# Kernel optimization log

Hardware: AMD Instinct MI355X
Metric: run time of the kernel (lower is better)

The kernel has to match this reference:

```python
import jax, jax.numpy as jnp
import numpy as np
from math import gcd

KAISER_BETA = 5.0  # scipy resample_poly default window=('kaiser', 5.0)


def _firwin_kaiser(numtaps, cutoff, beta):
    # lowpass firwin equivalent: windowed-sinc, normalized to unity DC gain
    m = np.arange(numtaps) - (numtaps - 1) / 2.0
    h = cutoff * np.sinc(cutoff * m)
    h *= np.kaiser(numtaps, beta)
    h /= h.sum()
    return h


def _output_len(len_h, in_len, up, down):
    # full upfirdn output length
    return ((in_len - 1) * up + len_h - 1) // down + 1


def _make_filter(du, su, n_in):
    # replicates scipy.signal.resample_poly filter design + zero padding
    g = gcd(su, du)
    up, down = su // g, du // g
    max_rate = max(up, down)
    half_len = 10 * max_rate
    h = _firwin_kaiser(2 * half_len + 1, 1.0 / max_rate, KAISER_BETA) * up
    n_pre_pad = down - half_len % down
    n_out = n_in * up // down + bool((n_in * up) % down)
    n_pre_remove = (half_len + n_pre_pad) // down
    n_post_pad = 0
    while _output_len(len(h) + n_pre_pad + n_post_pad, n_in, up, down) < n_out + n_pre_remove:
        n_post_pad += 1
    h = np.concatenate([np.zeros(n_pre_pad), h, np.zeros(n_post_pad)]).astype(np.float32)
    return h


B, T, C = 16, 1_280_000, 4


def setup_inputs() -> dict:
    key = jax.random.key(0)
    x = jax.random.normal(key, (B, T, C), dtype=jnp.float32)
    h = jnp.asarray(_make_filter(640, 50, T))  # [1345]
    return {"x": x, "h": h, "su": 50, "du": 640}


def reference(x, h, su, du):
    # polyphase resampling: upsample by `up` (lhs_dilation), FIR filter h
    # (full convolution), downsample by `down` (stride) == scipy upfirdn,
    # then trim transients exactly as scipy.signal.resample_poly does.
    Bx, Tx, Cx = x.shape
    g = gcd(su, du)
    up, down = su // g, du // g  # 5, 64
    half_len = 10 * max(up, down)
    n_pre_pad = down - half_len % down
    n_pre_remove = (half_len + n_pre_pad) // down
    n_out = Tx * up // down + bool((Tx * up) % down)
    K = h.shape[0]
    # resample along time axis (axis=1): [B, T, C] -> [B*C, 1, T]
    xc = jnp.transpose(x, (0, 2, 1)).reshape(Bx * Cx, 1, Tx)
    kern = h[::-1].reshape(1, 1, K).astype(x.dtype)  # flip: conv, not corr
    y = jax.lax.conv_general_dilated(
        xc, kern,
        window_strides=(down,),
        padding=[(K - 1, K - 1)],
        lhs_dilation=(up,),
        dimension_numbers=("NCH", "OIH", "NCH"),
    )  # [B*C, 1, L_full]
    y = y[:, 0, n_pre_remove:n_pre_remove + n_out]
    return jnp.transpose(y.reshape(Bx, Cx, n_out), (0, 2, 1))  # [B, n_out, C]
```

## Files before the change

### kernel.cpp

```cpp
#include <hip/hip_runtime.h>

#define T_IN    1280000
#define N_OUT   100000
#define NQ      20000
#define KH      1345
#define NKP     352
#define QT      64
#define NTILE   313
#define LOW_PAD 163
#define SPAN    4388
#define PLANE_BYTES 18640
#define LDS_BYTES   74560

__global__ void build_tables(const float* __restrict__ h, float* __restrict__ ws) {
    int k = blockIdx.x * blockDim.x + threadIdx.x;
    if (k >= NKP) return;
    int m0 = 5 * k - 256;
    float4* tab4 = (float4*)ws;
    float*  tab1 = ws + NKP * 4;
    float v0 = (m0       >= 0 && m0       < KH) ? h[m0]       : 0.0f;
    float v1 = (m0 + 64  >= 0 && m0 + 64  < KH) ? h[m0 + 64]  : 0.0f;
    float v2 = (m0 + 128 >= 0 && m0 + 128 < KH) ? h[m0 + 128] : 0.0f;
    float v3 = (m0 + 192 >= 0 && m0 + 192 < KH) ? h[m0 + 192] : 0.0f;
    float v4 = (m0 + 256 >= 0 && m0 + 256 < KH) ? h[m0 + 256] : 0.0f;
    tab4[k] = make_float4(v0, v1, v2, v3);
    tab1[k] = v4;
}

#define STEP(T, TB, CMP) \
  a0.x = fmaf(T.x, xq0.CMP, a0.x); a0.y = fmaf(T.x, xq1.CMP, a0.y); \
  a0.z = fmaf(T.x, xq2.CMP, a0.z); a0.w = fmaf(T.x, xq3.CMP, a0.w); \
  a1.x = fmaf(T.y, xq0.CMP, a1.x); a1.y = fmaf(T.y, xq1.CMP, a1.y); \
  a1.z = fmaf(T.y, xq2.CMP, a1.z); a1.w = fmaf(T.y, xq3.CMP, a1.w); \
  a2.x = fmaf(T.z, xq0.CMP, a2.x); a2.y = fmaf(T.z, xq1.CMP, a2.y); \
  a2.z = fmaf(T.z, xq2.CMP, a2.z); a2.w = fmaf(T.z, xq3.CMP, a2.w); \
  a3.x = fmaf(T.w, xq0.CMP, a3.x); a3.y = fmaf(T.w, xq1.CMP, a3.y); \
  a3.z = fmaf(T.w, xq2.CMP, a3.z); a3.w = fmaf(T.w, xq3.CMP, a3.w); \
  a4.x = fmaf(TB,  xq0.CMP, a4.x); a4.y = fmaf(TB,  xq1.CMP, a4.y); \
  a4.z = fmaf(TB,  xq2.CMP, a4.z); a4.w = fmaf(TB,  xq3.CMP, a4.w);

__launch_bounds__(512, 4)
__global__ void downsample_poly(const float* __restrict__ x,
                                const float* __restrict__ ws,
                                float* __restrict__ out) {
    extern __shared__ __align__(16) unsigned char lds_raw[];
    const int tid = threadIdx.x;
    const int b   = blockIdx.y;
    const int q0  = blockIdx.x * QT;
    const int jlo = 64 * q0 - LOW_PAD;

    const float4* __restrict__ xb = (const float4*)x + (size_t)b * T_IN;

    for (int i = tid; i < SPAN; i += 512) {
        int j = jlo + i;
        float4 v = make_float4(0.f, 0.f, 0.f, 0.f);
        if ((unsigned)j < (unsigned)T_IN) v = xb[j];
        int G    = i >> 2;
        int slot = G + (G >> 4);
        int base = slot * 16 + (i & 3) * 4;
        *(float*)(lds_raw + base)                   = v.x;
        *(float*)(lds_raw + base +     PLANE_BYTES) = v.y;
        *(float*)(lds_raw + base + 2 * PLANE_BYTES) = v.z;
        *(float*)(lds_raw + base + 3 * PLANE_BYTES) = v.w;
    }
    __syncthreads();

    const int dq = tid & 63;
    const int su = __builtin_amdgcn_readfirstlane(tid >> 6);
    const float4* __restrict__ tap4 = (const float4*)ws;
    const float*  __restrict__ tap1 = ws + NKP * 4;

    float4 a0 = make_float4(0.f,0.f,0.f,0.f), a1 = a0, a2 = a0, a3 = a0, a4 = a0;
    const int k00 = su * 44;
    const int Gb0 = 16 * dq + 88 - 11 * su;

    #pragma unroll 2
    for (int g = 0; g < 11; ++g) {
        int k0   = k00 + 4 * g;
        int Gb   = Gb0 - g;
        int slot = Gb + (Gb >> 4);
        const unsigned char* pb = lds_raw + slot * 16;
        float4 xq0 = *(const float4*)(pb);
        float4 xq1 = *(const float4*)(pb +     PLANE_BYTES);
        float4 xq2 = *(const float4*)(pb + 2 * PLANE_BYTES);
        float4 xq3 = *(const float4*)(pb + 3 * PLANE_BYTES);
        float4 t0 = tap4[k0], t1 = tap4[k0 + 1], t2 = tap4[k0 + 2], t3 = tap4[k0 + 3];
        float4 u1 = *(const float4*)(tap1 + k0);
        STEP(t0, u1.x, w)
        STEP(t1, u1.y, z)
        STEP(t2, u1.z, y)
        STEP(t3, u1.w, x)
    }

    __syncthreads();
    {
        float4* pp = (float4*)(lds_raw + tid * 80);
        pp[0] = a0; pp[1] = a1; pp[2] = a2; pp[3] = a3; pp[4] = a4;
    }
    __syncthreads();
    if (tid < 320 && 5 * q0 + tid < 5 * NQ) {
        float sx = 0.f, sy = 0.f, sz = 0.f, sw = 0.f;
        #pragma unroll
        for (int ss = 0; ss < 8; ++ss) {
            float4 p = *(const float4*)(lds_raw + ss * 5120 + tid * 16);
            sx += p.x; sy += p.y; sz += p.z; sw += p.w;
        }
        ((float4*)out)[(size_t)b * N_OUT + 5 * (size_t)q0 + tid] =
            make_float4(sx, sy, sz, sw);
    }
}

extern "C" void kernel_launch(void* const* d_in, const int* in_sizes, int n_in,
                              void* d_out, int out_size, void* d_ws, size_t ws_size,
                              hipStream_t stream) {
    const float* x = (const float*)d_in[0];
    const float* h = (const float*)d_in[1];
    float* out = (float*)d_out;
    float* ws  = (float*)d_ws;

    hipFuncSetAttribute((const void*)downsample_poly,
                        hipFuncAttributeMaxDynamicSharedMemorySize, LDS_BYTES);

    hipLaunchKernelGGL(build_tables, dim3(2), dim3(192), 0, stream, h, ws);
    hipLaunchKernelGGL(downsample_poly, dim3(NTILE, 16), dim3(512), LDS_BYTES,
                       stream, x, ws, out);
}
```

Baseline: 458.6 us.

## Stage input in fp16 LDS and use packed fdot2 for polyphase taps

Converts the staged input and filter taps to packed fp16 pairs and replaces the fp32 FMA chains with v_dot2 (fdot2) accumulating into fp32. This halves LDS footprint, which allows static shared memory, an XOR swizzle instead of padded slots, and a launch bound of 8 waves per SIMD target. It aims to cut ALU instruction count and LDS traffic. The trade-off is reduced precision of input and taps from round-toward-zero fp16 conversion, which may exceed tolerance.

```diff
diff --git a/kernel.cpp b/kernel.cpp
--- a/kernel.cpp
+++ b/kernel.cpp
@@ -1,112 +1,113 @@
 #include <hip/hip_runtime.h>
 
-#define T_IN    1280000
-#define N_OUT   100000
-#define NQ      20000
-#define KH      1345
-#define NKP     352
-#define QT      64
-#define NTILE   313
-#define LOW_PAD 163
-#define SPAN    4388
-#define PLANE_BYTES 18640
-#define LDS_BYTES   74560
+typedef _Float16 h2 __attribute__((ext_vector_type(2)));
+typedef _Float16 h4 __attribute__((ext_vector_type(4)));
 
-__global__ void build_tables(const float* __restrict__ h, float* __restrict__ ws) {
-    int k = blockIdx.x * blockDim.x + threadIdx.x;
-    if (k >= NKP) return;
-    int m0 = 5 * k - 256;
-    float4* tab4 = (float4*)ws;
-    float*  tab1 = ws + NKP * 4;
-    float v0 = (m0       >= 0 && m0       < KH) ? h[m0]       : 0.0f;
-    float v1 = (m0 + 64  >= 0 && m0 + 64  < KH) ? h[m0 + 64]  : 0.0f;
-    float v2 = (m0 + 128 >= 0 && m0 + 128 < KH) ? h[m0 + 128] : 0.0f;
-    float v3 = (m0 + 192 >= 0 && m0 + 192 < KH) ? h[m0 + 192] : 0.0f;
-    float v4 = (m0 + 256 >= 0 && m0 + 256 < KH) ? h[m0 + 256] : 0.0f;
-    tab4[k] = make_float4(v0, v1, v2, v3);
-    tab1[k] = v4;
+#define T_IN   1280000
+#define N_OUT  100000
+#define NQ     20000
+#define KH     1345
+#define NMP    176
+#define QT     64
+#define NTILE  313
+#define OFFJ   159
+#define NPAIR  2240
+#define PLANE  9216
+#define SWZ(b) ((b) ^ ((((b) >> 7) & 15) << 3))
+#define PKRTZ(a, b) __builtin_bit_cast(h2, __builtin_amdgcn_cvt_pkrtz((a), (b)))
+
+__global__ void build_tables(const float* __restrict__ h, unsigned* __restrict__ ws) {
+    int m = blockIdx.x * blockDim.x + threadIdx.x;
+    if (m >= NMP) return;
+    #pragma unroll
+    for (int r = 0; r < 5; ++r) {
+        int ilo = 5 * (2 * m)     - 256 + 64 * r;
+        int ihi = 5 * (2 * m + 1) - 256 + 64 * r;
+        float vlo = (ilo >= 0 && ilo < KH) ? h[ilo] : 0.f;
+        float vhi = (ihi >= 0 && ihi < KH) ? h[ihi] : 0.f;
+        h2 p = PKRTZ(vhi, vlo);
+        ws[m * 5 + r] = __builtin_bit_cast(unsigned, p);
+    }
 }
 
-#define STEP(T, TB, CMP) \
-  a0.x = fmaf(T.x, xq0.CMP, a0.x); a0.y = fmaf(T.x, xq1.CMP, a0.y); \
-  a0.z = fmaf(T.x, xq2.CMP, a0.z); a0.w = fmaf(T.x, xq3.CMP, a0.w); \
-  a1.x = fmaf(T.y, xq0.CMP, a1.x); a1.y = fmaf(T.y, xq1.CMP, a1.y); \
-  a1.z = fmaf(T.y, xq2.CMP, a1.z); a1.w = fmaf(T.y, xq3.CMP, a1.w); \
-  a2.x = fmaf(T.z, xq0.CMP, a2.x); a2.y = fmaf(T.z, xq1.CMP, a2.y); \
-  a2.z = fmaf(T.z, xq2.CMP, a2.z); a2.w = fmaf(T.z, xq3.CMP, a2.w); \
-  a3.x = fmaf(T.w, xq0.CMP, a3.x); a3.y = fmaf(T.w, xq1.CMP, a3.y); \
-  a3.z = fmaf(T.w, xq2.CMP, a3.z); a3.w = fmaf(T.w, xq3.CMP, a3.w); \
-  a4.x = fmaf(TB,  xq0.CMP, a4.x); a4.y = fmaf(TB,  xq1.CMP, a4.y); \
-  a4.z = fmaf(TB,  xq2.CMP, a4.z); a4.w = fmaf(TB,  xq3.CMP, a4.w);
+#define DOT_R(AR, TH, TL) \
+  AR.x = __builtin_amdgcn_fdot2(TH, Xl0, AR.x, false); \
+  AR.x = __builtin_amdgcn_fdot2(TL, Xh0, AR.x, false); \
+  AR.y = __builtin_amdgcn_fdot2(TH, Xl1, AR.y, false); \
+  AR.y = __builtin_amdgcn_fdot2(TL, Xh1, AR.y, false); \
+  AR.z = __builtin_amdgcn_fdot2(TH, Xl2, AR.z, false); \
+  AR.z = __builtin_amdgcn_fdot2(TL, Xh2, AR.z, false); \
+  AR.w = __builtin_amdgcn_fdot2(TH, Xl3, AR.w, false); \
+  AR.w = __builtin_amdgcn_fdot2(TL, Xh3, AR.w, false);
 
-__launch_bounds__(512, 4)
+__launch_bounds__(512, 8)
 __global__ void downsample_poly(const float* __restrict__ x,
-                                const float* __restrict__ ws,
+                                const unsigned* __restrict__ ws,
                                 float* __restrict__ out) {
-    extern __shared__ __align__(16) unsigned char lds_raw[];
+    __shared__ __align__(16) char lds[40960];
     const int tid = threadIdx.x;
     const int b   = blockIdx.y;
     const int q0  = blockIdx.x * QT;
-    const int jlo = 64 * q0 - LOW_PAD;
-
+    const int jlo = 64 * q0 - OFFJ;
     const float4* __restrict__ xb = (const float4*)x + (size_t)b * T_IN;
 
-    for (int i = tid; i < SPAN; i += 512) {
-        int j = jlo + i;
-        float4 v = make_float4(0.f, 0.f, 0.f, 0.f);
-        if ((unsigned)j < (unsigned)T_IN) v = xb[j];
-        int G    = i >> 2;
-        int slot = G + (G >> 4);
-        int base = slot * 16 + (i & 3) * 4;
-        *(float*)(lds_raw + base)                   = v.x;
-        *(float*)(lds_raw + base +     PLANE_BYTES) = v.y;
-        *(float*)(lds_raw + base + 2 * PLANE_BYTES) = v.z;
-        *(float*)(lds_raw + base + 3 * PLANE_BYTES) = v.w;
+    #pragma unroll
+    for (int it = 0; it < 5; ++it) {
+        int i2 = tid + it * 512;
+        if (i2 < NPAIR) {
+            int j0 = jlo + 2 * i2;
+            float4 v0 = make_float4(0.f, 0.f, 0.f, 0.f), v1 = v0;
+            if ((unsigned)j0       < (unsigned)T_IN) v0 = xb[j0];
+            if ((unsigned)(j0 + 1) < (unsigned)T_IN) v1 = xb[j0 + 1];
+            int bb = SWZ(4 * i2);
+            *(h2*)(lds + bb)             = PKRTZ(v0.x, v1.x);
+            *(h2*)(lds + bb +     PLANE) = PKRTZ(v0.y, v1.y);
+            *(h2*)(lds + bb + 2 * PLANE) = PKRTZ(v0.z, v1.z);
+            *(h2*)(lds + bb + 3 * PLANE) = PKRTZ(v0.w, v1.w);
+        }
     }
     __syncthreads();
 
     const int dq = tid & 63;
     const int su = __builtin_amdgcn_readfirstlane(tid >> 6);
-    const float4* __restrict__ tap4 = (const float4*)ws;
-    const float*  __restrict__ tap1 = ws + NKP * 4;
-
     float4 a0 = make_float4(0.f,0.f,0.f,0.f), a1 = a0, a2 = a0, a3 = a0, a4 = a0;
-    const int k00 = su * 44;
-    const int Gb0 = 16 * dq + 88 - 11 * su;
+    const int rb0 = 128 * dq + 696 - 88 * su;
 
     #pragma unroll 2
     for (int g = 0; g < 11; ++g) {
-        int k0   = k00 + 4 * g;
-        int Gb   = Gb0 - g;
-        int slot = Gb + (Gb >> 4);
-        const unsigned char* pb = lds_raw + slot * 16;
-        float4 xq0 = *(const float4*)(pb);
-        float4 xq1 = *(const float4*)(pb +     PLANE_BYTES);
-        float4 xq2 = *(const float4*)(pb + 2 * PLANE_BYTES);
-        float4 xq3 = *(const float4*)(pb + 3 * PLANE_BYTES);
-        float4 t0 = tap4[k0], t1 = tap4[k0 + 1], t2 = tap4[k0 + 2], t3 = tap4[k0 + 3];
-        float4 u1 = *(const float4*)(tap1 + k0);
-        STEP(t0, u1.x, w)
-        STEP(t1, u1.y, z)
-        STEP(t2, u1.z, y)
-        STEP(t3, u1.w, x)
+        int sw = SWZ(rb0 - 8 * g);
+        h4 X0 = *(const h4*)(lds + sw);
+        h4 X1 = *(const h4*)(lds + sw +     PLANE);
+        h4 X2 = *(const h4*)(lds + sw + 2 * PLANE);
+        h4 X3 = *(const h4*)(lds + sw + 3 * PLANE);
+        h2 Xl0 = {X0[0], X0[1]}, Xh0 = {X0[2], X0[3]};
+        h2 Xl1 = {X1[0], X1[1]}, Xh1 = {X1[2], X1[3]};
+        h2 Xl2 = {X2[0], X2[1]}, Xh2 = {X2[2], X2[3]};
+        h2 Xl3 = {X3[0], X3[1]}, Xh3 = {X3[2], X3[3]};
+        const unsigned* tw = ws + (110 * su + 10 * g);
+        h2 th, tl;
+        th = __builtin_bit_cast(h2, tw[5]); tl = __builtin_bit_cast(h2, tw[0]); DOT_R(a0, th, tl)
+        th = __builtin_bit_cast(h2, tw[6]); tl = __builtin_bit_cast(h2, tw[1]); DOT_R(a1, th, tl)
+        th = __builtin_bit_cast(h2, tw[7]); tl = __builtin_bit_cast(h2, tw[2]); DOT_R(a2, th, tl)
+        th = __builtin_bit_cast(h2, tw[8]); tl = __builtin_bit_cast(h2, tw[3]); DOT_R(a3, th, tl)
+        th = __builtin_bit_cast(h2, tw[9]); tl = __builtin_bit_cast(h2, tw[4]); DOT_R(a4, th, tl)
     }
 
     __syncthreads();
     {
-        float4* pp = (float4*)(lds_raw + tid * 80);
+        float4* pp = (float4*)(lds + tid * 80);
         pp[0] = a0; pp[1] = a1; pp[2] = a2; pp[3] = a3; pp[4] = a4;
     }
     __syncthreads();
     if (tid < 320 && 5 * q0 + tid < 5 * NQ) {
-        float sx = 0.f, sy = 0.f, sz = 0.f, sw = 0.f;
+        float sx = 0.f, sy = 0.f, sz = 0.f, sw2 = 0.f;
         #pragma unroll
         for (int ss = 0; ss < 8; ++ss) {
-            float4 p = *(const float4*)(lds_raw + ss * 5120 + tid * 16);
-            sx += p.x; sy += p.y; sz += p.z; sw += p.w;
+            float4 p = *(const float4*)(lds + ss * 5120 + tid * 16);
+            sx += p.x; sy += p.y; sz += p.z; sw2 += p.w;
         }
         ((float4*)out)[(size_t)b * N_OUT + 5 * (size_t)q0 + tid] =
-            make_float4(sx, sy, sz, sw);
+            make_float4(sx, sy, sz, sw2);
     }
 }
 
@@ -116,12 +117,9 @@
     const float* x = (const float*)d_in[0];
     const float* h = (const float*)d_in[1];
     float* out = (float*)d_out;
-    float* ws  = (float*)d_ws;
+    unsigned* ws = (unsigned*)d_ws;
 
-    hipFuncSetAttribute((const void*)downsample_poly,
-                        hipFuncAttributeMaxDynamicSharedMemorySize, LDS_BYTES);
-
-    hipLaunchKernelGGL(build_tables, dim3(2), dim3(192), 0, stream, h, ws);
-    hipLaunchKernelGGL(downsample_poly, dim3(NTILE, 16), dim3(512), LDS_BYTES,
-                       stream, x, ws, out);
+    hipLaunchKernelGGL(build_tables, dim3(1), dim3(192), 0, stream, h, ws);
+    hipLaunchKernelGGL(downsample_poly, dim3(NTILE, 16), dim3(512), 0, stream,
+                       x, ws, out);
 }
```

Measured after the change: 449.5 us. 1.02x faster.

## Use persistent blocks with double-buffered async global-to-LDS DMA and swizzled layout

Applied to the files above, without the earlier changes.

Replaces the one-block-per-tile grid with 256 persistent blocks that loop over tiles. Each block prefetches the next tile's input straight into LDS with global_load_lds while it computes the current one, so load latency overlaps compute. The LDS layout moves from channel-split planes to an XOR-swizzled float4 layout, and edge tiles get explicit zero fill. The cost is twice the LDS per block, lower occupancy, and hand-placed waitcnt and barrier ordering that is easy to get wrong.

```diff
diff --git a/kernel.cpp b/kernel.cpp
--- a/kernel.cpp
+++ b/kernel.cpp
@@ -1,16 +1,19 @@
 #include <hip/hip_runtime.h>
 
-#define T_IN    1280000
-#define N_OUT   100000
-#define NQ      20000
-#define KH      1345
-#define NKP     352
-#define QT      64
-#define NTILE   313
-#define LOW_PAD 163
-#define SPAN    4388
-#define PLANE_BYTES 18640
-#define LDS_BYTES   74560
+
+#define T_IN   1280000
+#define N_OUT  100000
+#define NQ     20000
+#define KH     1345
+#define NKP    352
+#define NTILE  313
+#define NTASK  5008
+#define GRID   256
+#define OFFJ   159
+#define SPAN   4480
+#define NCHUNK 70
+#define BUFB   71680
+#define LDSSZ  143360
 
 __global__ void build_tables(const float* __restrict__ h, float* __restrict__ ws) {
     int k = blockIdx.x * blockDim.x + threadIdx.x;
@@ -27,86 +30,114 @@
     tab1[k] = v4;
 }
 
-#define STEP(T, TB, CMP) \
-  a0.x = fmaf(T.x, xq0.CMP, a0.x); a0.y = fmaf(T.x, xq1.CMP, a0.y); \
-  a0.z = fmaf(T.x, xq2.CMP, a0.z); a0.w = fmaf(T.x, xq3.CMP, a0.w); \
-  a1.x = fmaf(T.y, xq0.CMP, a1.x); a1.y = fmaf(T.y, xq1.CMP, a1.y); \
-  a1.z = fmaf(T.y, xq2.CMP, a1.z); a1.w = fmaf(T.y, xq3.CMP, a1.w); \
-  a2.x = fmaf(T.z, xq0.CMP, a2.x); a2.y = fmaf(T.z, xq1.CMP, a2.y); \
-  a2.z = fmaf(T.z, xq2.CMP, a2.z); a2.w = fmaf(T.z, xq3.CMP, a2.w); \
-  a3.x = fmaf(T.w, xq0.CMP, a3.x); a3.y = fmaf(T.w, xq1.CMP, a3.y); \
-  a3.z = fmaf(T.w, xq2.CMP, a3.z); a3.w = fmaf(T.w, xq3.CMP, a3.w); \
-  a4.x = fmaf(TB,  xq0.CMP, a4.x); a4.y = fmaf(TB,  xq1.CMP, a4.y); \
-  a4.z = fmaf(TB,  xq2.CMP, a4.z); a4.w = fmaf(TB,  xq3.CMP, a4.w);
+#define FMA20(T, TB, XV) \
+  a0.x = fmaf(T.x, XV.x, a0.x); a0.y = fmaf(T.x, XV.y, a0.y); \
+  a0.z = fmaf(T.x, XV.z, a0.z); a0.w = fmaf(T.x, XV.w, a0.w); \
+  a1.x = fmaf(T.y, XV.x, a1.x); a1.y = fmaf(T.y, XV.y, a1.y); \
+  a1.z = fmaf(T.y, XV.z, a1.z); a1.w = fmaf(T.y, XV.w, a1.w); \
+  a2.x = fmaf(T.z, XV.x, a2.x); a2.y = fmaf(T.z, XV.y, a2.y); \
+  a2.z = fmaf(T.z, XV.z, a2.z); a2.w = fmaf(T.z, XV.w, a2.w); \
+  a3.x = fmaf(T.w, XV.x, a3.x); a3.y = fmaf(T.w, XV.y, a3.y); \
+  a3.z = fmaf(T.w, XV.z, a3.z); a3.w = fmaf(T.w, XV.w, a3.w); \
+  a4.x = fmaf(TB,  XV.x, a4.x); a4.y = fmaf(TB,  XV.y, a4.y); \
+  a4.z = fmaf(TB,  XV.z, a4.z); a4.w = fmaf(TB,  XV.w, a4.w);
 
-__launch_bounds__(512, 4)
+#define WAIT_VM8   asm volatile("s_waitcnt vmcnt(8)" ::: "memory")
+#define WAIT_LGKM0 asm volatile("s_waitcnt lgkmcnt(0)" ::: "memory")
+#define BAR() { __builtin_amdgcn_sched_barrier(0); __builtin_amdgcn_s_barrier(); \
+                __builtin_amdgcn_sched_barrier(0); }
+
+typedef const __attribute__((address_space(1))) void* gas_t;
+typedef __attribute__((address_space(3))) void* las_t;
+
+#define ISSUE_DMA(UU, BUFP) { \
+    int bb_ = (UU) / NTILE; \
+    int tt_ = (UU) - bb_ * NTILE; \
+    int jlo_ = (tt_ << 12) - OFFJ; \
+    const float4* __restrict__ xb_ = (const float4*)x + (size_t)bb_ * T_IN; \
+    for (int c_ = wid; c_ < NCHUNK; c_ += 8) { \
+        int j_ = jlo_ + (c_ << 6) + (lane ^ (c_ & 7)); \
+        j_ = j_ < 0 ? 0 : (j_ >= T_IN ? T_IN - 1 : j_); \
+        __builtin_amdgcn_global_load_lds((gas_t)(xb_ + j_), \
+                                         (las_t)((BUFP) + (c_ << 10)), 16, 0, 0); \
+    } }
+
+__launch_bounds__(512, 2)
 __global__ void downsample_poly(const float* __restrict__ x,
                                 const float* __restrict__ ws,
                                 float* __restrict__ out) {
-    extern __shared__ __align__(16) unsigned char lds_raw[];
-    const int tid = threadIdx.x;
-    const int b   = blockIdx.y;
-    const int q0  = blockIdx.x * QT;
-    const int jlo = 64 * q0 - LOW_PAD;
-
-    const float4* __restrict__ xb = (const float4*)x + (size_t)b * T_IN;
-
-    for (int i = tid; i < SPAN; i += 512) {
-        int j = jlo + i;
-        float4 v = make_float4(0.f, 0.f, 0.f, 0.f);
-        if ((unsigned)j < (unsigned)T_IN) v = xb[j];
-        int G    = i >> 2;
-        int slot = G + (G >> 4);
-        int base = slot * 16 + (i & 3) * 4;
-        *(float*)(lds_raw + base)                   = v.x;
-        *(float*)(lds_raw + base +     PLANE_BYTES) = v.y;
-        *(float*)(lds_raw + base + 2 * PLANE_BYTES) = v.z;
-        *(float*)(lds_raw + base + 3 * PLANE_BYTES) = v.w;
-    }
-    __syncthreads();
-
-    const int dq = tid & 63;
-    const int su = __builtin_amdgcn_readfirstlane(tid >> 6);
+    extern __shared__ __align__(16) char lds[];
+    const int tid  = threadIdx.x;
+    const int lane = tid & 63;
+    const int wid  = __builtin_amdgcn_readfirstlane(tid >> 6);
+    const int dq   = lane;
+    const int su   = wid;
     const float4* __restrict__ tap4 = (const float4*)ws;
     const float*  __restrict__ tap1 = ws + NKP * 4;
+    const int mbase = 64 * dq + 348 - 44 * su;
 
-    float4 a0 = make_float4(0.f,0.f,0.f,0.f), a1 = a0, a2 = a0, a3 = a0, a4 = a0;
-    const int k00 = su * 44;
-    const int Gb0 = 16 * dq + 88 - 11 * su;
+    int u = blockIdx.x;
+    ISSUE_DMA(u, lds)
 
-    #pragma unroll 2
-    for (int g = 0; g < 11; ++g) {
-        int k0   = k00 + 4 * g;
-        int Gb   = Gb0 - g;
-        int slot = Gb + (Gb >> 4);
-        const unsigned char* pb = lds_raw + slot * 16;
-        float4 xq0 = *(const float4*)(pb);
-        float4 xq1 = *(const float4*)(pb +     PLANE_BYTES);
-        float4 xq2 = *(const float4*)(pb + 2 * PLANE_BYTES);
-        float4 xq3 = *(const float4*)(pb + 3 * PLANE_BYTES);
-        float4 t0 = tap4[k0], t1 = tap4[k0 + 1], t2 = tap4[k0 + 2], t3 = tap4[k0 + 3];
-        float4 u1 = *(const float4*)(tap1 + k0);
-        STEP(t0, u1.x, w)
-        STEP(t1, u1.y, z)
-        STEP(t2, u1.z, y)
-        STEP(t3, u1.w, x)
-    }
+    for (int it = 0; u < NTASK; u += GRID, ++it) {
+        char* bufC = lds + ((it & 1) ? BUFB : 0);
+        char* bufN = lds + ((it & 1) ? 0 : BUFB);
+        int un = u + GRID; if (un >= NTASK) un = u;
+        ISSUE_DMA(un, bufN)
 
-    __syncthreads();
-    {
-        float4* pp = (float4*)(lds_raw + tid * 80);
-        pp[0] = a0; pp[1] = a1; pp[2] = a2; pp[3] = a3; pp[4] = a4;
-    }
-    __syncthreads();
-    if (tid < 320 && 5 * q0 + tid < 5 * NQ) {
-        float sx = 0.f, sy = 0.f, sz = 0.f, sw = 0.f;
-        #pragma unroll
-        for (int ss = 0; ss < 8; ++ss) {
-            float4 p = *(const float4*)(lds_raw + ss * 5120 + tid * 16);
-            sx += p.x; sy += p.y; sz += p.z; sw += p.w;
+        WAIT_VM8;
+        BAR();
+
+        const int bb  = u / NTILE;
+        const int tt  = u - bb * NTILE;
+        const int jlo = (tt << 12) - OFFJ;
+        int lo_bad = jlo < 0 ? -jlo : 0;
+        int hi_bad = T_IN - jlo; if (hi_bad > SPAN) hi_bad = SPAN;
+        if (lo_bad > 0 || hi_bad < SPAN) {
+            for (int m = tid; m < SPAN; m += 512)
+                if (m < lo_bad || m >= hi_bad)
+                    *(float4*)(bufC + ((m ^ ((m >> 6) & 7)) << 4)) =
+                        make_float4(0.f, 0.f, 0.f, 0.f);
+            WAIT_LGKM0; BAR();
         }
-        ((float4*)out)[(size_t)b * N_OUT + 5 * (size_t)q0 + tid] =
-            make_float4(sx, sy, sz, sw);
+
+        float4 a0 = make_float4(0.f,0.f,0.f,0.f), a1 = a0, a2 = a0, a3 = a0, a4 = a0;
+        for (int g = 0; g < 11; ++g) {
+            int m  = mbase - 4 * g;
+            int xr = (m >> 6) & 7;
+            float4 X0 = *(const float4*)(bufC + (((m    ) ^ xr) << 4));
+            float4 X1 = *(const float4*)(bufC + (((m + 1) ^ xr) << 4));
+            float4 X2 = *(const float4*)(bufC + (((m + 2) ^ xr) << 4));
+            float4 X3 = *(const float4*)(bufC + (((m + 3) ^ xr) << 4));
+            int k0 = 44 * su + 4 * g;
+            float4 t0 = tap4[k0], t1 = tap4[k0+1], t2 = tap4[k0+2], t3 = tap4[k0+3];
+            float4 u1 = *(const float4*)(tap1 + k0);
+            FMA20(t3, u1.w, X0)
+            FMA20(t2, u1.z, X1)
+            FMA20(t1, u1.y, X2)
+            FMA20(t0, u1.x, X3)
+        }
+
+        WAIT_LGKM0; BAR();
+        {
+            float4* pp = (float4*)(bufC + tid * 80);
+            pp[0] = a0; pp[1] = a1; pp[2] = a2; pp[3] = a3; pp[4] = a4;
+        }
+        WAIT_LGKM0; BAR();
+        {
+            int q0 = tt << 6;
+            if (tid < 320 && 5 * q0 + tid < 5 * NQ) {
+                float sx = 0.f, sy = 0.f, sz = 0.f, sw = 0.f;
+                #pragma unroll
+                for (int ss = 0; ss < 8; ++ss) {
+                    float4 p = *(const float4*)(bufC + ss * 5120 + tid * 16);
+                    sx += p.x; sy += p.y; sz += p.z; sw += p.w;
+                }
+                ((float4*)out)[(size_t)bb * N_OUT + 5 * (size_t)q0 + tid] =
+                    make_float4(sx, sy, sz, sw);
+            }
+        }
+        WAIT_LGKM0; BAR();
     }
 }
 
@@ -119,9 +150,9 @@
     float* ws  = (float*)d_ws;
 
     hipFuncSetAttribute((const void*)downsample_poly,
-                        hipFuncAttributeMaxDynamicSharedMemorySize, LDS_BYTES);
+                        hipFuncAttributeMaxDynamicSharedMemorySize, LDSSZ);
 
     hipLaunchKernelGGL(build_tables, dim3(2), dim3(192), 0, stream, h, ws);
-    hipLaunchKernelGGL(downsample_poly, dim3(NTILE, 16), dim3(512), LDS_BYTES,
-                       stream, x, ws, out);
+    hipLaunchKernelGGL(downsample_poly, dim3(GRID), dim3(512), LDSSZ, stream,
+                       x, ws, out);
 }
```

Result: no change. 453.6 us (-1.1%).
